# Kernel optimization log

Hardware: AMD Instinct MI355X
Metric: run time of the kernel (lower is better)

## Reference

```python
import jax, jax.numpy as jnp
import numpy as np

B, NQ, D, NH, L, P = 8, 1000, 256, 8, 4, 4
DFF = 1024
HD = D // NH
SHAPES = np.array([[128, 128], [64, 64], [32, 32], [16, 16]], dtype=np.int64)
S = int((SHAPES[:, 0] * SHAPES[:, 1]).sum())  # 21760
LEVEL_START = np.concatenate([np.zeros(1, np.int64), np.cumsum(SHAPES[:, 0] * SHAPES[:, 1])[:-1]])


def setup_inputs() -> dict:
    key = jax.random.key(0)
    ks = jax.random.split(key, 20)
    w = lambda k, shape, s=0.02: jax.random.normal(k, shape, jnp.float32) * s
    z = lambda n: jnp.zeros((n,), jnp.float32)
    return dict(
        query=w(ks[0], (B, NQ, D), 1.0),
        query_pos=w(ks[1], (B, NQ, D), 1.0),
        reference_points=jax.random.uniform(ks[2], (B, NQ, L, 4), jnp.float32),
        input_flatten=w(ks[3], (B, S, D), 1.0),
        input_spatial_shapes=SHAPES,
        input_level_start_index=LEVEL_START,
        Wq=w(ks[4], (D, D)), bq=z(D), Wk=w(ks[5], (D, D)), bk=z(D),
        Wv=w(ks[6], (D, D)), bv=z(D), Wo=w(ks[7], (D, D)), bo=z(D),
        ln1_g=jnp.ones((D,), jnp.float32), ln1_b=z(D),
        W_off=w(ks[8], (D, NH * L * P * 2)), b_off=z(NH * L * P * 2),
        W_attn=w(ks[9], (D, NH * L * P)), b_attn=z(NH * L * P),
        W_val=w(ks[10], (D, D)), b_val=z(D),
        W_cout=w(ks[11], (D, D)), b_cout=z(D),
        ln2_g=jnp.ones((D,), jnp.float32), ln2_b=z(D),
        W1=w(ks[12], (D, DFF)), b1=z(DFF),
        W2=w(ks[13], (DFF, D)), b2=z(D),
        ln3_g=jnp.ones((D,), jnp.float32), ln3_b=z(D),
    )


def layer_norm(x, g, b, eps=1e-5):
    mu = x.mean(-1, keepdims=True)
    var = ((x - mu) ** 2).mean(-1, keepdims=True)
    return (x - mu) / jnp.sqrt(var + eps) * g + b


def _ms_deform(value, shapes_np, loc, aw):
    # value: (B,S,NH,HD); loc: (B,Nq,NH,L,P,2) in [0,1]; aw: (B,Nq,NH,L,P)
    Bz, _, nh, hd = value.shape
    Nq = loc.shape[1]
    awt = aw.transpose(0, 2, 1, 3, 4)  # (B,NH,Nq,L,P)
    acc = jnp.zeros((Bz, nh, Nq, hd), value.dtype)
    start = 0
    for lvl in range(shapes_np.shape[0]):
        Hl, Wl = int(shapes_np[lvl, 0]), int(shapes_np[lvl, 1])
        vf = value[:, start:start + Hl * Wl].transpose(0, 2, 1, 3)  # (B,NH,Hl*Wl,HD)
        start += Hl * Wl
        # grid_sample align_corners=False: pixel coord = loc * size - 0.5
        lx = loc[:, :, :, lvl, :, 0].transpose(0, 2, 1, 3) * Wl - 0.5  # (B,NH,Nq,P)
        ly = loc[:, :, :, lvl, :, 1].transpose(0, 2, 1, 3) * Hl - 0.5
        x0 = jnp.floor(lx); y0 = jnp.floor(ly)
        tx = lx - x0; ty = ly - y0
        x0i = x0.astype(jnp.int32); y0i = y0.astype(jnp.int32)

        def gather(xi, yi):
            valid = (xi >= 0) & (xi < Wl) & (yi >= 0) & (yi < Hl)
            idx = jnp.clip(yi, 0, Hl - 1) * Wl + jnp.clip(xi, 0, Wl - 1)
            out = jnp.take_along_axis(vf, idx.reshape(Bz, nh, Nq * P)[..., None], axis=2)
            return out.reshape(Bz, nh, Nq, P, hd) * valid[..., None]

        g00 = gather(x0i, y0i)
        g01 = gather(x0i + 1, y0i)
        g10 = gather(x0i, y0i + 1)
        g11 = gather(x0i + 1, y0i + 1)
        samp = (g00 * ((1 - tx) * (1 - ty))[..., None] + g01 * (tx * (1 - ty))[..., None]
                + g10 * ((1 - tx) * ty)[..., None] + g11 * (tx * ty)[..., None])  # (B,NH,Nq,P,HD)
        acc = acc + jnp.einsum('bhqp,bhqpd->bhqd', awt[:, :, :, lvl], samp)
    return acc.transpose(0, 2, 1, 3).reshape(Bz, Nq, nh * hd)


def reference(query, query_pos, reference_points, input_flatten, input_spatial_shapes,
              input_level_start_index, Wq, bq, Wk, bk, Wv, bv, Wo, bo, ln1_g, ln1_b,
              W_off, b_off, W_attn, b_attn, W_val, b_val, W_cout, b_cout, ln2_g, ln2_b,
              W1, b1, W2, b2, ln3_g, ln3_b):
    Bz, Nq, Dm = query.shape
    # --- self-attention (post-norm), pos added to Q/K only ---
    qp = query + query_pos
    q = (qp @ Wq + bq).reshape(Bz, Nq, NH, HD)
    k = (qp @ Wk + bk).reshape(Bz, Nq, NH, HD)
    v = (query @ Wv + bv).reshape(Bz, Nq, NH, HD)
    att = jax.nn.softmax(jnp.einsum('bqhd,bkhd->bhqk', q, k) / jnp.sqrt(jnp.float32(HD)), axis=-1)
    sa = jnp.einsum('bhqk,bkhd->bqhd', att, v).reshape(Bz, Nq, Dm) @ Wo + bo
    x = layer_norm(query + sa, ln1_g, ln1_b)
    # --- deformable cross-attention ---
    q2 = x + query_pos
    value = (input_flatten @ W_val + b_val).reshape(Bz, -1, NH, HD)
    off = (q2 @ W_off + b_off).reshape(Bz, Nq, NH, L, P, 2)
    aw = jax.nn.softmax((q2 @ W_attn + b_attn).reshape(Bz, Nq, NH, L * P), axis=-1)
    aw = aw.reshape(Bz, Nq, NH, L, P)
    rp = reference_points  # (B,Nq,L,4) cxcywh
    loc = rp[:, :, None, :, None, :2] + off / P * rp[:, :, None, :, None, 2:] * 0.5
    shapes_np = np.asarray(input_spatial_shapes)
    ca = _ms_deform(value, shapes_np, loc, aw) @ W_cout + b_cout
    x = layer_norm(x + ca, ln2_g, ln2_b)
    # --- FFN ---
    ffn = jax.nn.relu(x @ W1 + b1) @ W2 + b2
    return layer_norm(x + ffn, ln3_g, ln3_b)
```

## Files before the change

kernel.cpp:

```cpp
#include <hip/hip_runtime.h>
#include <hip/hip_bf16.h>

#define B_   8
#define NQ_  1000
#define D_   256
#define NH_  8
#define L_   4
#define P_   4
#define DFF_ 1024
#define HD_  32
#define S_   21760
#define NTOK (B_*NQ_)

typedef short  bf16x8 __attribute__((ext_vector_type(8)));
typedef float  f32x4  __attribute__((ext_vector_type(4)));

#define WAITBAR(N) asm volatile("s_waitcnt vmcnt(" #N ") lgkmcnt(0)\n\ts_barrier" ::: "memory")
#define ENDBAR()   asm volatile("s_barrier" ::: "memory")

__device__ inline unsigned short f32_to_bf16_bits(float f) {
    unsigned int u = __float_as_uint(f);
    unsigned int rounding = 0x7FFFu + ((u >> 16) & 1u);
    u += rounding;
    return (unsigned short)(u >> 16);
}
__device__ inline float bf16_bits_to_f32(unsigned short b) {
    return __uint_as_float(((unsigned int)b) << 16);
}
__device__ inline unsigned int pack_trunc(float f0, float f1) {
    return __builtin_amdgcn_perm(__float_as_uint(f1), __float_as_uint(f0), 0x07060302u);
}
__device__ inline void async_copy16(const void* g, void* l) {
    __builtin_amdgcn_global_load_lds((const __attribute__((address_space(1))) unsigned int*)g,
                                     (__attribute__((address_space(3))) unsigned int*)l, 16, 0, 0);
}

struct PrepArgs {
    const float* wsrc[10];
    unsigned short* wdst[10];
    int wK[10], wN[10];
    const float* bq; const float* bk; const float* boff; const float* battn;
    float* qkb; float* oab;
    const float* input_flat; unsigned short* if_bf;
    const float* query; const float* qpos;
    unsigned short* q_bf; unsigned short* qp_bf;
};
__global__ __launch_bounds__(256) void prep_k(PrepArgs P)
{
    const int bid = blockIdx.x, tid = threadIdx.x;
    if (bid < 640) {
        const int job = bid >> 6, tile = bid & 63;
        const int K = P.wK[job], N = P.wN[job];
        const int tilesN = N >> 6;
        if (tile >= (K >> 6) * tilesN) return;
        const int kt = tile / tilesN, nt = tile - kt * tilesN;
        const int k0 = kt * 64, n0 = nt * 64;
        __shared__ unsigned short t_[64][65];
        const float* src = P.wsrc[job];
        unsigned short* dst = P.wdst[job];
        const int cc = tid & 63, rr = tid >> 6;
        #pragma unroll
        for (int i = 0; i < 16; i++) {
            int k = i * 4 + rr;
            t_[k][cc] = f32_to_bf16_bits(src[(size_t)(k0 + k) * N + n0 + cc]);
        }
        __syncthreads();
        #pragma unroll
        for (int i = 0; i < 16; i++) {
            int n = i * 4 + rr;
            dst[(size_t)(n0 + n) * K + k0 + cc] = t_[cc][n];
        }
    } else if (bid < 2816) {
        const int base = (bid - 640) * 2560 + tid;
        float4 fr[10][2];
        #pragma unroll
        for (int i = 0; i < 10; i++) {
            const float* p = P.input_flat + (size_t)(base + i * 256) * 8;
            fr[i][0] = *reinterpret_cast<const float4*>(p);
            fr[i][1] = *reinterpret_cast<const float4*>(p + 4);
        }
        #pragma unroll
        for (int i = 0; i < 10; i++) {
            uint4 t;
            t.x = pack_trunc(fr[i][0].x, fr[i][0].y);
            t.y = pack_trunc(fr[i][0].z, fr[i][0].w);
            t.z = pack_trunc(fr[i][1].x, fr[i][1].y);
            t.w = pack_trunc(fr[i][1].z, fr[i][1].w);
            *reinterpret_cast<uint4*>(P.if_bf + (size_t)(base + i * 256) * 8) = t;
        }
    } else if (bid == 2816) {
        P.qkb[tid]       = P.bq[tid];
        P.qkb[256 + tid] = P.bk[tid];
        P.oab[tid]       = P.boff[tid];
        if (tid < 128) P.oab[256 + tid] = P.battn[tid];
    } else {
        const int base = (bid - 2817) * 1024 + tid;
        float4 fq[4][2], fp[4][2];
        #pragma unroll
        for (int i = 0; i < 4; i++) {
            const float* q = P.query + (size_t)(base + i * 256) * 8;
            const float* p = P.qpos  + (size_t)(base + i * 256) * 8;
            fq[i][0] = *reinterpret_cast<const float4*>(q);
            fq[i][1] = *reinterpret_cast<const float4*>(q + 4);
            fp[i][0] = *reinterpret_cast<const float4*>(p);
            fp[i][1] = *reinterpret_cast<const float4*>(p + 4);
        }
        #pragma unroll
        for (int i = 0; i < 4; i++) {
            uint4 tq, tp;
            tq.x = pack_trunc(fq[i][0].x, fq[i][0].y);
            tq.y = pack_trunc(fq[i][0].z, fq[i][0].w);
            tq.z = pack_trunc(fq[i][1].x, fq[i][1].y);
            tq.w = pack_trunc(fq[i][1].z, fq[i][1].w);
            tp.x = pack_trunc(fq[i][0].x + fp[i][0].x, fq[i][0].y + fp[i][0].y);
            tp.y = pack_trunc(fq[i][0].z + fp[i][0].z, fq[i][0].w + fp[i][0].w);
            tp.z = pack_trunc(fq[i][1].x + fp[i][1].x, fq[i][1].y + fp[i][1].y);
            tp.w = pack_trunc(fq[i][1].z + fp[i][1].z, fq[i][1].w + fp[i][1].w);
            *reinterpret_cast<uint4*>(P.q_bf  + (size_t)(base + i * 256) * 8) = tq;
            *reinterpret_cast<uint4*>(P.qp_bf + (size_t)(base + i * 256) * 8) = tp;
        }
    }
}

__global__ __launch_bounds__(256) void vgemm0(const unsigned short* __restrict__ Ab,
                                              const unsigned short* __restrict__ Bt,
                                              const float* __restrict__ bias,
                                              unsigned short* __restrict__ Cb)
{
    constexpr int K = 256;
    constexpr int N = 256;
    __shared__ __align__(16) unsigned short sA[2][128 * 64];
    __shared__ __align__(16) unsigned short sB[2][128 * 64];
    const int tid = threadIdx.x;
    const int w = tid >> 6, l = tid & 63;
    const int n0 = blockIdx.x * 128, m0 = blockIdx.y * 128;
    const int wr = w >> 1, wc = w & 1;

    f32x4 acc[4][4];
    #pragma unroll
    for (int i = 0; i < 4; i++)
        #pragma unroll
        for (int j = 0; j < 4; j++)
            #pragma unroll
            for (int r = 0; r < 4; r++) acc[i][j][r] = 0.f;

    auto issueA = [&](int t, int buf) {
        #pragma unroll
        for (int r = 0; r < 4; r++) {
            int boff = ((r * 4 + w) * 64 + l) * 16;
            int row  = boff >> 7;
            int kb   = (boff & 127) ^ ((row & 7) << 4);
            async_copy16(Ab + (size_t)(m0 + row) * K + t * 64 + (kb >> 1),
                         sA[buf] + (size_t)(r * 4 + w) * 512);
        }
    };
    auto issueB = [&](int t, int buf) {
        #pragma unroll
        for (int r = 0; r < 4; r++) {
            int boff = ((r * 4 + w) * 64 + l) * 16;
            int row  = boff >> 7;
            int kb   = (boff & 127) ^ ((row & 7) << 4);
            async_copy16(Bt + (size_t)(n0 + row) * K + t * 64 + (kb >> 1),
                         sB[buf] + (size_t)(r * 4 + w) * 512);
        }
    };

    issueA(0, 0);
    issueB(0, 0);

    for (int t = 0; t < 4; t++) {
        const int cur = t & 1;
        if (t + 1 < 4) {
            issueA(t + 1, cur ^ 1);
            issueB(t + 1, cur ^ 1);
            WAITBAR(8);
        } else {
            WAITBAR(0);
        }
        #pragma unroll
        for (int kk = 0; kk < 2; kk++) {
            bf16x8 afr[4], bfr[4];
            const int kbyte = kk * 64 + ((l >> 4) << 4);
            #pragma unroll
            for (int mi = 0; mi < 4; mi++) {
                int row = wr * 64 + mi * 16 + (l & 15);
                int sw = kbyte ^ ((row & 7) << 4);
                afr[mi] = *reinterpret_cast<const bf16x8*>(&sA[cur][row * 64 + (sw >> 1)]);
            }
            #pragma unroll
            for (int ni = 0; ni < 4; ni++) {
                int row = wc * 64 + ni * 16 + (l & 15);
                int sw = kbyte ^ ((row & 7) << 4);
                bfr[ni] = *reinterpret_cast<const bf16x8*>(&sB[cur][row * 64 + (sw >> 1)]);
            }
            #pragma unroll
            for (int mi = 0; mi < 4; mi++)
                #pragma unroll
                for (int ni = 0; ni < 4; ni++)
                    acc[mi][ni] = __builtin_amdgcn_mfma_f32_16x16x32_bf16(
                        afr[mi], bfr[ni], acc[mi][ni], 0, 0, 0);
        }
        ENDBAR();
    }

    #pragma unroll
    for (int mi = 0; mi < 4; mi++) {
        #pragma unroll
        for (int ni = 0; ni < 4; ni++) {
            int col = n0 + wc * 64 + ni * 16 + (l & 15);
            float bz = bias[col];
            #pragma unroll
            for (int rg = 0; rg < 4; rg++) {
                int row = m0 + wr * 64 + mi * 16 + ((l >> 4) << 2) + rg;
                Cb[(size_t)row * N + col] = f32_to_bf16_bits(acc[mi][ni][rg] + bz);
            }
        }
    }
}

template<bool RELU, int CMODE, int BN, int K>
__global__ __launch_bounds__(256) void bgemm(const unsigned short* __restrict__ Ab,
                                             const unsigned short* __restrict__ Bt,
                                             const float* __restrict__ bias,
                                             float* __restrict__ Cf,
                                             unsigned short* __restrict__ Cb,
                                             int N)
{
    constexpr int NF   = BN / 16;
    constexpr int KF   = K / 32;
    constexpr int ROWB = K * 2;
    constexpr int FILL = BN * ROWB / 4096;

    __shared__ __align__(16) unsigned short sB[BN * K];

    const int tid = threadIdx.x;
    const int w = tid >> 6, l = tid & 63;
    const int g = l >> 4, lr = l & 15;
    const int n0 = blockIdx.x * BN;

    #pragma unroll
    for (int r = 0; r < FILL; r++) {
        int lin = (r * 256 + tid) * 16;
        int row = lin / ROWB;
        int kb  = (lin & (ROWB - 1)) ^ ((row & 7) << 4);
        async_copy16(Bt + (size_t)(n0 + row) * K + (kb >> 1), (char*)sB + lin);
    }
    asm volatile("s_waitcnt vmcnt(0)\n\ts_barrier" ::: "memory");

    float bz[NF];
    #pragma unroll
    for (int nf = 0; nf < NF; nf++) bz[nf] = bias[n0 + nf * 16 + lr];

    const int m0w = blockIdx.y * 64 + w * 16;
    const int arow = m0w + lr;

    f32x4 acc[NF];
    #pragma unroll
    for (int nf = 0; nf < NF; nf++)
        #pragma unroll
        for (int r = 0; r < 4; r++) acc[nf][r] = 0.f;

    #pragma unroll
    for (int kf = 0; kf < KF; kf++) {
        bf16x8 af = *reinterpret_cast<const bf16x8*>(Ab + (size_t)arow * K + kf * 32 + g * 8);
        #pragma unroll
        for (int nf = 0; nf < NF; nf++) {
            int brow = nf * 16 + lr;
            bf16x8 bf = *reinterpret_cast<const bf16x8*>(
                (const char*)sB + brow * ROWB + ((kf * 64 + g * 16) ^ ((brow & 7) << 4)));
            acc[nf] = __builtin_amdgcn_mfma_f32_16x16x32_bf16(af, bf, acc[nf], 0, 0, 0);
        }
    }

    #pragma unroll
    for (int nf = 0; nf < NF; nf++) {
        int col = n0 + nf * 16 + lr;
        if constexpr (CMODE == 2) {
            int row0 = m0w + g * 4;
            int bb = row0 / 1000;
            int key = row0 - bb * 1000;
            ushort4 q4;
            q4.x = f32_to_bf16_bits(acc[nf][0] + bz[nf]);
            q4.y = f32_to_bf16_bits(acc[nf][1] + bz[nf]);
            q4.z = f32_to_bf16_bits(acc[nf][2] + bz[nf]);
            q4.w = f32_to_bf16_bits(acc[nf][3] + bz[nf]);
            *reinterpret_cast<ushort4*>(Cb + (size_t)bb * 262144 + (size_t)col * 1024 + key) = q4;
        } else {
            #pragma unroll
            for (int rg = 0; rg < 4; rg++) {
                int row = m0w + g * 4 + rg;
                float v = acc[nf][rg] + bz[nf];
                if (RELU) v = fmaxf(v, 0.f);
                if constexpr (CMODE == 1)
                    Cb[(size_t)row * N + col] = f32_to_bf16_bits(v);
                else
                    Cf[(size_t)row * N + col] = v;
            }
        }
    }
}

__global__ __launch_bounds__(256) void fattn_k(const unsigned short* __restrict__ qk,
                                               const unsigned short* __restrict__ vt,
                                               unsigned short* __restrict__ sa)
{
    const int b = blockIdx.z, h = blockIdx.y;
    const int tid = threadIdx.x;
    const int w = tid >> 6, l = tid & 63;
    const int lq = l & 15, g = l >> 4;
    const int q0 = blockIdx.x * 64 + w * 16;

    __shared__ __align__(16) unsigned short Ks[2][128 * 32];
    __shared__ __align__(16) unsigned short Vs[2][32 * 128];
    __shared__ __align__(16) unsigned short Ps[4][16 * 128];

    int qrow = q0 + lq; if (qrow > NQ_ - 1) qrow = NQ_ - 1;
    const bf16x8 qfrag = *reinterpret_cast<const bf16x8*>(
        qk + ((size_t)(b * NQ_ + qrow)) * 512 + h * 32 + g * 8);

    f32x4 O0 = {0.f, 0.f, 0.f, 0.f}, O1 = {0.f, 0.f, 0.f, 0.f};
    float m = -1e30f, lsum = 0.f;
    const float scale = 0.17677669529663687f;

    const size_t kbase = (size_t)b * (NQ_ * 512) + 256 + h * 32;
    const size_t vbase = (size_t)b * 262144 + (size_t)(h * 32) * 1024;
    const int swz = (lq & 7) << 4;

    auto issueKV = [&](int kt, int buf) {
        #pragma unroll
        for (int r = 0; r < 2; r++) {
            int lin = (r * 256 + tid) * 16;
            int krow = lin >> 6;
            int kb = (lin & 63) ^ ((krow & 7) << 4);
            async_copy16(qk + kbase + (size_t)(kt * 128 + krow) * 512 + (kb >> 1),
                         (char*)Ks[buf] + lin);
            int d = lin >> 8;
            int vb = (lin & 255) ^ ((d & 7) << 4);
            async_copy16(vt + vbase + (size_t)d * 1024 + kt * 128 + (vb >> 1),
                         (char*)Vs[buf] + lin);
        }
    };

    issueKV(0, 0);

    for (int kt = 0; kt < 8; kt++) {
        const int k0 = kt * 128;
        const int cur = kt & 1;
        asm volatile("s_waitcnt vmcnt(0) lgkmcnt(0)\n\ts_barrier" ::: "memory");
        if (kt < 7) issueKV(kt + 1, cur ^ 1);

        const unsigned short* Kc = Ks[cur];
        const unsigned short* Vc = Vs[cur];

        float t[8][4];
        float tmax = -1e30f;
        const bool tail = (k0 + 128 > NQ_);
        #pragma unroll
        for (int ni = 0; ni < 8; ni++) {
            int row = ni * 16 + lq;
            bf16x8 kf = *reinterpret_cast<const bf16x8*>(
                (const char*)Kc + row * 64 + ((g * 16) ^ swz));
            f32x4 st = __builtin_amdgcn_mfma_f32_16x16x32_bf16(
                kf, qfrag, (f32x4){0.f, 0.f, 0.f, 0.f}, 0, 0, 0);
            #pragma unroll
            for (int rg = 0; rg < 4; rg++) {
                float tv = st[rg] * scale;
                if (tail) {
                    int key = k0 + ni * 16 + g * 4 + rg;
                    tv = (key < NQ_) ? tv : -1e30f;
                }
                t[ni][rg] = tv;
                tmax = fmaxf(tmax, tv);
            }
        }
        tmax = fmaxf(tmax, __shfl_xor(tmax, 16));
        tmax = fmaxf(tmax, __shfl_xor(tmax, 32));
        float mnew = fmaxf(m, tmax);
        float corr = __expf(m - mnew);
        m = mnew;

        float rs = 0.f;
        unsigned int pk[8][2];
        #pragma unroll
        for (int ni = 0; ni < 8; ni++) {
            float p0 = __expf(t[ni][0] - mnew);
            float p1 = __expf(t[ni][1] - mnew);
            float p2 = __expf(t[ni][2] - mnew);
            float p3 = __expf(t[ni][3] - mnew);
            rs += (p0 + p1) + (p2 + p3);
            pk[ni][0] = ((unsigned)f32_to_bf16_bits(p0)) | (((unsigned)f32_to_bf16_bits(p1)) << 16);
            pk[ni][1] = ((unsigned)f32_to_bf16_bits(p2)) | (((unsigned)f32_to_bf16_bits(p3)) << 16);
        }
        rs += __shfl_xor(rs, 16);
        rs += __shfl_xor(rs, 32);
        lsum = lsum * corr + rs;

        float c0 = __shfl(corr, g * 4 + 0);
        float c1 = __shfl(corr, g * 4 + 1);
        float c2 = __shfl(corr, g * 4 + 2);
        float c3 = __shfl(corr, g * 4 + 3);
        O0[0] *= c0; O0[1] *= c1; O0[2] *= c2; O0[3] *= c3;
        O1[0] *= c0; O1[1] *= c1; O1[2] *= c2; O1[3] *= c3;

        unsigned short* Pw = Ps[w];
        #pragma unroll
        for (int ni = 0; ni < 8; ni++) {
            int byteoff = lq * 256 + ((ni * 32 + g * 8) ^ swz);
            *reinterpret_cast<uint2*>((char*)Pw + byteoff) = make_uint2(pk[ni][0], pk[ni][1]);
        }

        #pragma unroll
        for (int c = 0; c < 4; c++) {
            int rb = (c * 64 + g * 16) ^ swz;
            bf16x8 pa = *reinterpret_cast<const bf16x8*>((const char*)Pw + lq * 256 + rb);
            bf16x8 v0 = *reinterpret_cast<const bf16x8*>((const char*)Vc + lq * 256 + rb);
            bf16x8 v1 = *reinterpret_cast<const bf16x8*>((const char*)Vc + (16 + lq) * 256 + rb);
            O0 = __builtin_amdgcn_mfma_f32_16x16x32_bf16(pa, v0, O0, 0, 0, 0);
            O1 = __builtin_amdgcn_mfma_f32_16x16x32_bf16(pa, v1, O1, 0, 0, 0);
        }
    }

    float linv = 1.f / lsum;
    float i0 = __shfl(linv, g * 4 + 0);
    float i1 = __shfl(linv, g * 4 + 1);
    float i2 = __shfl(linv, g * 4 + 2);
    float i3 = __shfl(linv, g * 4 + 3);
    float iv[4] = {i0, i1, i2, i3};
    #pragma unroll
    for (int rg = 0; rg < 4; rg++) {
        int qg = q0 + g * 4 + rg;
        if (qg < NQ_) {
            size_t obase = ((size_t)(b * NQ_ + qg)) * 256 + h * 32;
            sa[obase + lq]      = f32_to_bf16_bits(O0[rg] * iv[rg]);
            sa[obase + 16 + lq] = f32_to_bf16_bits(O1[rg] * iv[rg]);
        }
    }
}

template<int OM>
__global__ __launch_bounds__(256) void ln_k(const float* __restrict__ a,
                                            const float* __restrict__ bsum,
                                            const float* __restrict__ pos,
                                            const float* __restrict__ g,
                                            const float* __restrict__ be,
                                            float* __restrict__ out,
                                            unsigned short* __restrict__ outb)
{
    const int wave = threadIdx.x >> 6, lane = threadIdx.x & 63;
    const int row = blockIdx.x * 4 + wave;
    float4 xa = reinterpret_cast<const float4*>(a + (size_t)row * 256)[lane];
    float4 xb = reinterpret_cast<const float4*>(bsum + (size_t)row * 256)[lane];
    float4 x = {xa.x + xb.x, xa.y + xb.y, xa.z + xb.z, xa.w + xb.w};
    float s  = x.x + x.y + x.z + x.w;
    float ss = x.x * x.x + x.y * x.y + x.z * x.z + x.w * x.w;
    #pragma unroll
    for (int off = 32; off > 0; off >>= 1) {
        s  += __shfl_xor(s, off);
        ss += __shfl_xor(ss, off);
    }
    float mu  = s * (1.f / 256.f);
    float var = ss * (1.f / 256.f) - mu * mu;
    float rstd = rsqrtf(var + 1e-5f);
    float4 gv = reinterpret_cast<const float4*>(g)[lane];
    float4 bv = reinterpret_cast<const float4*>(be)[lane];
    float4 o = {(x.x - mu) * rstd * gv.x + bv.x,
                (x.y - mu) * rstd * gv.y + bv.y,
                (x.z - mu) * rstd * gv.z + bv.z,
                (x.w - mu) * rstd * gv.w + bv.w};
    reinterpret_cast<float4*>(out + (size_t)row * 256)[lane] = o;
    if constexpr (OM == 1) {
        ushort4 q4;
        q4.x = f32_to_bf16_bits(o.x); q4.y = f32_to_bf16_bits(o.y);
        q4.z = f32_to_bf16_bits(o.z); q4.w = f32_to_bf16_bits(o.w);
        *reinterpret_cast<ushort4*>(outb + (size_t)row * 256 + lane * 4) = q4;
    } else if constexpr (OM == 2) {
        float4 pv = reinterpret_cast<const float4*>(pos + (size_t)row * 256)[lane];
        ushort4 q4;
        q4.x = f32_to_bf16_bits(o.x + pv.x); q4.y = f32_to_bf16_bits(o.y + pv.y);
        q4.z = f32_to_bf16_bits(o.z + pv.z); q4.w = f32_to_bf16_bits(o.w + pv.w);
        *reinterpret_cast<ushort4*>(outb + (size_t)row * 256 + lane * 4) = q4;
    }
}

__device__ inline unsigned int samp2(const unsigned short* __restrict__ v,
                                     int b, int st, int Wl, int Hl,
                                     int x, int y, int hc)
{
    bool valid = (x >= 0) & (x < Wl) & (y >= 0) & (y < Hl);
    int xc = min(max(x, 0), Wl - 1);
    int yc = min(max(y, 0), Hl - 1);
    size_t idx = ((size_t)(b * S_ + st + yc * Wl + xc)) * 256 + hc;
    unsigned int val = *reinterpret_cast<const unsigned int*>(v + idx);
    return valid ? val : 0u;
}

__global__ __launch_bounds__(256) void deform_k(const float* __restrict__ rp,
                                                const float* __restrict__ oa,
                                                const unsigned short* __restrict__ value,
                                                unsigned short* __restrict__ ca)
{
    const int tk = threadIdx.x >> 7;
    const int tok = blockIdx.x * 2 + tk;
    const int b = tok / NQ_;
    const int h = (threadIdx.x >> 4) & 7;
    const int cp = threadIdx.x & 15;
    const int hc = h * 32 + cp * 2;

    const float* awp = oa + (size_t)tok * 384 + 256 + h * 16;
    float w[16];
    float mx = -1e30f;
    #pragma unroll
    for (int i = 0; i < 16; i++) { w[i] = awp[i]; mx = fmaxf(mx, w[i]); }
    float sum = 0.f;
    #pragma unroll
    for (int i = 0; i < 16; i++) { w[i] = __expf(w[i] - mx); sum += w[i]; }
    const float inv = 1.f / sum;

    const float* rpp  = rp + (size_t)tok * (L_ * 4);
    const float* offp = oa + (size_t)tok * 384 + h * 32;

    const int lvlW[4] = {128, 64, 32, 16};
    const int lvlS[4] = {0, 16384, 20480, 21504};

    float acc0 = 0.f, acc1 = 0.f;
    #pragma unroll
    for (int l = 0; l < 4; l++) {
        const int Wl = lvlW[l], Hl = lvlW[l], st = lvlS[l];
        const float cx = rpp[l * 4 + 0], cy = rpp[l * 4 + 1];
        const float cw = rpp[l * 4 + 2], chh = rpp[l * 4 + 3];
        #pragma unroll
        for (int p = 0; p < 4; p++) {
            float ox = offp[l * 8 + p * 2 + 0];
            float oy = offp[l * 8 + p * 2 + 1];
            float lx = (cx + ox * 0.25f * cw * 0.5f) * Wl - 0.5f;
            float ly = (cy + oy * 0.25f * chh * 0.5f) * Hl - 0.5f;
            float x0f = floorf(lx), y0f = floorf(ly);
            float tx = lx - x0f, ty = ly - y0f;
            int x0 = (int)x0f, y0 = (int)y0f;
            unsigned int u00 = samp2(value, b, st, Wl, Hl, x0,     y0,     hc);
            unsigned int u01 = samp2(value, b, st, Wl, Hl, x0 + 1, y0,     hc);
            unsigned int u10 = samp2(value, b, st, Wl, Hl, x0,     y0 + 1, hc);
            unsigned int u11 = samp2(value, b, st, Wl, Hl, x0 + 1, y0 + 1, hc);
            float w00 = (1.f - tx) * (1.f - ty), w01 = tx * (1.f - ty);
            float w10 = (1.f - tx) * ty,         w11 = tx * ty;
            float g0 = bf16_bits_to_f32((unsigned short)u00) * w00
                     + bf16_bits_to_f32((unsigned short)u01) * w01
                     + bf16_bits_to_f32((unsigned short)u10) * w10
                     + bf16_bits_to_f32((unsigned short)u11) * w11;
            float g1 = bf16_bits_to_f32((unsigned short)(u00 >> 16)) * w00
                     + bf16_bits_to_f32((unsigned short)(u01 >> 16)) * w01
                     + bf16_bits_to_f32((unsigned short)(u10 >> 16)) * w10
                     + bf16_bits_to_f32((unsigned short)(u11 >> 16)) * w11;
            float wa = w[l * 4 + p] * inv;
            acc0 += wa * g0;
            acc1 += wa * g1;
        }
    }
    unsigned int packed = ((unsigned)f32_to_bf16_bits(acc0)) | (((unsigned)f32_to_bf16_bits(acc1)) << 16);
    *reinterpret_cast<unsigned int*>(ca + (size_t)tok * 256 + hc) = packed;
}

extern "C" void kernel_launch(void* const* d_in, const int* in_sizes, int n_in,
                              void* d_out, int out_size, void* d_ws, size_t ws_size,
                              hipStream_t stream)
{
    const float* query      = (const float*)d_in[0];
    const float* query_pos  = (const float*)d_in[1];
    const float* ref_pts    = (const float*)d_in[2];
    const float* input_flat = (const float*)d_in[3];
    const float* Wq = (const float*)d_in[6];  const float* bq = (const float*)d_in[7];
    const float* Wk = (const float*)d_in[8];  const float* bk = (const float*)d_in[9];
    const float* Wv = (const float*)d_in[10]; const float* bv = (const float*)d_in[11];
    const float* Wo = (const float*)d_in[12]; const float* bo = (const float*)d_in[13];
    const float* ln1g = (const float*)d_in[14]; const float* ln1b = (const float*)d_in[15];
    const float* W_off = (const float*)d_in[16]; const float* b_off = (const float*)d_in[17];
    const float* W_attn = (const float*)d_in[18]; const float* b_attn = (const float*)d_in[19];
    const float* W_val = (const float*)d_in[20]; const float* b_val = (const float*)d_in[21];
    const float* W_cout = (const float*)d_in[22]; const float* b_cout = (const float*)d_in[23];
    const float* ln2g = (const float*)d_in[24]; const float* ln2b = (const float*)d_in[25];
    const float* W1 = (const float*)d_in[26]; const float* b1 = (const float*)d_in[27];
    const float* W2 = (const float*)d_in[28]; const float* b2 = (const float*)d_in[29];
    const float* ln3g = (const float*)d_in[30]; const float* ln3b = (const float*)d_in[31];
    float* out = (float*)d_out;

    char* base = (char*)d_ws;
    size_t off = 0;
    auto alloc = [&](size_t bytes) { void* p = base + off; off += (bytes + 255) & ~(size_t)255; return p; };
    unsigned short* value_bf = (unsigned short*)alloc((size_t)B_ * S_ * 256 * 2);
    unsigned short* if_bf = (unsigned short*)alloc((size_t)B_ * S_ * 256 * 2);
    unsigned short* qk_bf = (unsigned short*)alloc((size_t)NTOK * 1024 * 2);
    unsigned short* h_bf = qk_bf;
    unsigned short* vt = (unsigned short*)alloc((size_t)B_ * 256 * 1024 * 2);
    float* oa_buf = (float*)alloc((size_t)NTOK * 384 * 4);
    float* tmp0   = (float*)alloc((size_t)NTOK * 256 * 4);
    float* x1     = (float*)alloc((size_t)NTOK * 256 * 4);
    float* x2     = (float*)alloc((size_t)NTOK * 256 * 4);
    unsigned short* sc_bf  = (unsigned short*)alloc((size_t)NTOK * 256 * 2);
    unsigned short* q_bf   = (unsigned short*)alloc((size_t)NTOK * 256 * 2);
    unsigned short* qp_bf  = (unsigned short*)alloc((size_t)NTOK * 256 * 2);
    unsigned short* x1p_bf = (unsigned short*)alloc((size_t)NTOK * 256 * 2);
    unsigned short* x2_bf  = (unsigned short*)alloc((size_t)NTOK * 256 * 2);
    unsigned short* wqk   = (unsigned short*)alloc(512 * 256 * 2);
    unsigned short* wv    = (unsigned short*)alloc(256 * 256 * 2);
    unsigned short* wo    = (unsigned short*)alloc(256 * 256 * 2);
    unsigned short* woa   = (unsigned short*)alloc(384 * 256 * 2);
    unsigned short* wval  = (unsigned short*)alloc(256 * 256 * 2);
    unsigned short* wcout = (unsigned short*)alloc(256 * 256 * 2);
    unsigned short* w1t   = (unsigned short*)alloc(1024 * 256 * 2);
    unsigned short* w2t   = (unsigned short*)alloc(256 * 1024 * 2);
    float* qkbias = (float*)alloc(512 * 4);
    float* oabias = (float*)alloc(384 * 4);

    dim3 blk(256);

    PrepArgs P;
    P.wsrc[0] = Wq;    P.wdst[0] = wqk;               P.wK[0] = 256;  P.wN[0] = 256;
    P.wsrc[1] = Wk;    P.wdst[1] = wqk + 256 * 256;   P.wK[1] = 256;  P.wN[1] = 256;
    P.wsrc[2] = Wv;    P.wdst[2] = wv;                P.wK[2] = 256;  P.wN[2] = 256;
    P.wsrc[3] = Wo;    P.wdst[3] = wo;                P.wK[3] = 256;  P.wN[3] = 256;
    P.wsrc[4] = W_off; P.wdst[4] = woa;               P.wK[4] = 256;  P.wN[4] = 256;
    P.wsrc[5] = W_attn;P.wdst[5] = woa + 256 * 256;   P.wK[5] = 256;  P.wN[5] = 128;
    P.wsrc[6] = W_val; P.wdst[6] = wval;              P.wK[6] = 256;  P.wN[6] = 256;
    P.wsrc[7] = W_cout;P.wdst[7] = wcout;             P.wK[7] = 256;  P.wN[7] = 256;
    P.wsrc[8] = W1;    P.wdst[8] = w1t;               P.wK[8] = 256;  P.wN[8] = 1024;
    P.wsrc[9] = W2;    P.wdst[9] = w2t;               P.wK[9] = 1024; P.wN[9] = 256;
    P.bq = bq; P.bk = bk; P.boff = b_off; P.battn = b_attn;
    P.qkb = qkbias; P.oab = oabias;
    P.input_flat = input_flat; P.if_bf = if_bf;
    P.query = query; P.qpos = query_pos; P.q_bf = q_bf; P.qp_bf = qp_bf;
    prep_k<<<3067, blk, 0, stream>>>(P);

    bgemm<false, 1,  64, 256><<<dim3(8, 125), blk, 0, stream>>>(qp_bf, wqk, qkbias, nullptr, qk_bf, 512);
    bgemm<false, 2,  64, 256><<<dim3(4, 125), blk, 0, stream>>>(q_bf,  wv,  bv,     nullptr, vt,    256);
    fattn_k<<<dim3(16, NH_, B_), blk, 0, stream>>>(qk_bf, vt, sc_bf);
    bgemm<false, 0,  64, 256><<<dim3(4, 125), blk, 0, stream>>>(sc_bf, wo, bo, tmp0, nullptr, 256);
    ln_k<2><<<NTOK / 4, blk, 0, stream>>>(query, tmp0, query_pos, ln1g, ln1b, x1, x1p_bf);

    vgemm0<<<dim3(2, 1360), blk, 0, stream>>>(if_bf, wval, b_val, value_bf);
    bgemm<false, 0,  64, 256><<<dim3(6, 125), blk, 0, stream>>>(x1p_bf, woa, oabias, oa_buf, nullptr, 384);
    deform_k<<<NTOK / 2, blk, 0, stream>>>(ref_pts, oa_buf, value_bf, sc_bf);
    bgemm<false, 0,  64, 256><<<dim3(4, 125), blk, 0, stream>>>(sc_bf, wcout, b_cout, tmp0, nullptr, 256);
    ln_k<1><<<NTOK / 4, blk, 0, stream>>>(x1, tmp0, nullptr, ln2g, ln2b, x2, x2_bf);

    bgemm<true,  1,  64, 256><<<dim3(16, 125), blk, 0, stream>>>(x2_bf, w1t, b1, nullptr, h_bf, 1024);
    bgemm<false, 0,  32, 1024><<<dim3(8, 125), blk, 0, stream>>>(h_bf, w2t, b2, tmp0, nullptr, 256);
    ln_k<0><<<NTOK / 4, blk, 0, stream>>>(x2, tmp0, nullptr, ln3g, ln3b, out, nullptr);
}
```

Before: 276.0 us.

## Fuse fp32-to-bf16 conversion of input_flatten into the value-projection GEMM

Measured after the change: 253.7 us. -8.1%, faster.

```diff
diff --git a/kernel.cpp b/kernel.cpp
--- a/kernel.cpp
+++ b/kernel.cpp
@@ -41,7 +41,6 @@
     int wK[10], wN[10];
     const float* bq; const float* bk; const float* boff; const float* battn;
     float* qkb; float* oab;
-    const float* input_flat; unsigned short* if_bf;
     const float* query; const float* qpos;
     unsigned short* q_bf; unsigned short* qp_bf;
 };
@@ -70,31 +69,13 @@
             int n = i * 4 + rr;
             dst[(size_t)(n0 + n) * K + k0 + cc] = t_[cc][n];
         }
-    } else if (bid < 2816) {
-        const int base = (bid - 640) * 2560 + tid;
-        float4 fr[10][2];
-        #pragma unroll
-        for (int i = 0; i < 10; i++) {
-            const float* p = P.input_flat + (size_t)(base + i * 256) * 8;
-            fr[i][0] = *reinterpret_cast<const float4*>(p);
-            fr[i][1] = *reinterpret_cast<const float4*>(p + 4);
-        }
-        #pragma unroll
-        for (int i = 0; i < 10; i++) {
-            uint4 t;
-            t.x = pack_trunc(fr[i][0].x, fr[i][0].y);
-            t.y = pack_trunc(fr[i][0].z, fr[i][0].w);
-            t.z = pack_trunc(fr[i][1].x, fr[i][1].y);
-            t.w = pack_trunc(fr[i][1].z, fr[i][1].w);
-            *reinterpret_cast<uint4*>(P.if_bf + (size_t)(base + i * 256) * 8) = t;
-        }
-    } else if (bid == 2816) {
+    } else if (bid == 640) {
         P.qkb[tid]       = P.bq[tid];
         P.qkb[256 + tid] = P.bk[tid];
         P.oab[tid]       = P.boff[tid];
         if (tid < 128) P.oab[256 + tid] = P.battn[tid];
     } else {
-        const int base = (bid - 2817) * 1024 + tid;
+        const int base = (bid - 641) * 1024 + tid;
         float4 fq[4][2], fp[4][2];
         #pragma unroll
         for (int i = 0; i < 4; i++) {
@@ -122,19 +103,20 @@
     }
 }
 
-__global__ __launch_bounds__(256) void vgemm0(const unsigned short* __restrict__ Ab,
+__global__ __launch_bounds__(256) void vgemmF(const float* __restrict__ Af,
                                               const unsigned short* __restrict__ Bt,
                                               const float* __restrict__ bias,
                                               unsigned short* __restrict__ Cb)
 {
     constexpr int K = 256;
     constexpr int N = 256;
-    __shared__ __align__(16) unsigned short sA[2][128 * 64];
-    __shared__ __align__(16) unsigned short sB[2][128 * 64];
+    __shared__ __align__(16) float          sA[2][128 * 32];
+    __shared__ __align__(16) unsigned short sB[2][128 * 32];
     const int tid = threadIdx.x;
     const int w = tid >> 6, l = tid & 63;
     const int n0 = blockIdx.x * 128, m0 = blockIdx.y * 128;
     const int wr = w >> 1, wc = w & 1;
+    const int lq = l & 15, g = l >> 4;
 
     f32x4 acc[4][4];
     #pragma unroll
@@ -147,59 +129,64 @@
     auto issueA = [&](int t, int buf) {
         #pragma unroll
         for (int r = 0; r < 4; r++) {
-            int boff = ((r * 4 + w) * 64 + l) * 16;
-            int row  = boff >> 7;
-            int kb   = (boff & 127) ^ ((row & 7) << 4);
-            async_copy16(Ab + (size_t)(m0 + row) * K + t * 64 + (kb >> 1),
-                         sA[buf] + (size_t)(r * 4 + w) * 512);
+            int lin = (r * 256 + tid) * 16;
+            int row = lin >> 7;
+            int kb  = (lin & 127) ^ ((row & 3) << 5);
+            async_copy16(Af + (size_t)(m0 + row) * K + t * 32 + (kb >> 2),
+                         (char*)sA[buf] + lin);
         }
     };
     auto issueB = [&](int t, int buf) {
         #pragma unroll
-        for (int r = 0; r < 4; r++) {
-            int boff = ((r * 4 + w) * 64 + l) * 16;
-            int row  = boff >> 7;
-            int kb   = (boff & 127) ^ ((row & 7) << 4);
-            async_copy16(Bt + (size_t)(n0 + row) * K + t * 64 + (kb >> 1),
-                         sB[buf] + (size_t)(r * 4 + w) * 512);
+        for (int r = 0; r < 2; r++) {
+            int lin = (r * 256 + tid) * 16;
+            int row = lin >> 6;
+            int kb  = (lin & 63) ^ ((row & 3) << 4);
+            async_copy16(Bt + (size_t)(n0 + row) * K + t * 32 + (kb >> 1),
+                         (char*)sB[buf] + lin);
         }
     };
 
     issueA(0, 0);
     issueB(0, 0);
 
-    for (int t = 0; t < 4; t++) {
+    for (int t = 0; t < 8; t++) {
         const int cur = t & 1;
-        if (t + 1 < 4) {
+        if (t + 1 < 8) {
             issueA(t + 1, cur ^ 1);
             issueB(t + 1, cur ^ 1);
-            WAITBAR(8);
+            WAITBAR(6);
         } else {
             WAITBAR(0);
         }
-        #pragma unroll
-        for (int kk = 0; kk < 2; kk++) {
-            bf16x8 afr[4], bfr[4];
-            const int kbyte = kk * 64 + ((l >> 4) << 4);
+
+        bf16x8 afr[4], bfr[4];
+        #pragma unroll
+        for (int mi = 0; mi < 4; mi++) {
+            int row = wr * 64 + mi * 16 + lq;
+            int off = (g * 32) ^ ((row & 3) << 5);
+            const char* p = (const char*)sA[cur] + row * 128 + off;
+            float4 a0 = *reinterpret_cast<const float4*>(p);
+            float4 a1 = *reinterpret_cast<const float4*>(p + 16);
+            uint4 u;
+            u.x = pack_trunc(a0.x, a0.y);
+            u.y = pack_trunc(a0.z, a0.w);
+            u.z = pack_trunc(a1.x, a1.y);
+            u.w = pack_trunc(a1.z, a1.w);
+            afr[mi] = *reinterpret_cast<bf16x8*>(&u);
+        }
+        #pragma unroll
+        for (int ni = 0; ni < 4; ni++) {
+            int row = wc * 64 + ni * 16 + lq;
+            int off = (g * 16) ^ ((row & 3) << 4);
+            bfr[ni] = *reinterpret_cast<const bf16x8*>((const char*)sB[cur] + row * 64 + off);
+        }
+        #pragma unroll
+        for (int mi = 0; mi < 4; mi++)
             #pragma unroll
-            for (int mi = 0; mi < 4; mi++) {
-                int row = wr * 64 + mi * 16 + (l & 15);
-                int sw = kbyte ^ ((row & 7) << 4);
-                afr[mi] = *reinterpret_cast<const bf16x8*>(&sA[cur][row * 64 + (sw >> 1)]);
-            }
-            #pragma unroll
-            for (int ni = 0; ni < 4; ni++) {
-                int row = wc * 64 + ni * 16 + (l & 15);
-                int sw = kbyte ^ ((row & 7) << 4);
-                bfr[ni] = *reinterpret_cast<const bf16x8*>(&sB[cur][row * 64 + (sw >> 1)]);
-            }
-            #pragma unroll
-            for (int mi = 0; mi < 4; mi++)
-                #pragma unroll
-                for (int ni = 0; ni < 4; ni++)
-                    acc[mi][ni] = __builtin_amdgcn_mfma_f32_16x16x32_bf16(
-                        afr[mi], bfr[ni], acc[mi][ni], 0, 0, 0);
-        }
+            for (int ni = 0; ni < 4; ni++)
+                acc[mi][ni] = __builtin_amdgcn_mfma_f32_16x16x32_bf16(
+                    afr[mi], bfr[ni], acc[mi][ni], 0, 0, 0);
         ENDBAR();
     }
 
@@ -207,11 +194,11 @@
     for (int mi = 0; mi < 4; mi++) {
         #pragma unroll
         for (int ni = 0; ni < 4; ni++) {
-            int col = n0 + wc * 64 + ni * 16 + (l & 15);
+            int col = n0 + wc * 64 + ni * 16 + lq;
             float bz = bias[col];
             #pragma unroll
             for (int rg = 0; rg < 4; rg++) {
-                int row = m0 + wr * 64 + mi * 16 + ((l >> 4) << 2) + rg;
+                int row = m0 + wr * 64 + mi * 16 + g * 4 + rg;
                 Cb[(size_t)row * N + col] = f32_to_bf16_bits(acc[mi][ni][rg] + bz);
             }
         }
@@ -587,7 +574,6 @@
     size_t off = 0;
     auto alloc = [&](size_t bytes) { void* p = base + off; off += (bytes + 255) & ~(size_t)255; return p; };
     unsigned short* value_bf = (unsigned short*)alloc((size_t)B_ * S_ * 256 * 2);
-    unsigned short* if_bf = (unsigned short*)alloc((size_t)B_ * S_ * 256 * 2);
     unsigned short* qk_bf = (unsigned short*)alloc((size_t)NTOK * 1024 * 2);
     unsigned short* h_bf = qk_bf;
     unsigned short* vt = (unsigned short*)alloc((size_t)B_ * 256 * 1024 * 2);
@@ -626,9 +612,8 @@
     P.wsrc[9] = W2;    P.wdst[9] = w2t;               P.wK[9] = 1024; P.wN[9] = 256;
     P.bq = bq; P.bk = bk; P.boff = b_off; P.battn = b_attn;
     P.qkb = qkbias; P.oab = oabias;
-    P.input_flat = input_flat; P.if_bf = if_bf;
     P.query = query; P.qpos = query_pos; P.q_bf = q_bf; P.qp_bf = qp_bf;
-    prep_k<<<3067, blk, 0, stream>>>(P);
+    prep_k<<<891, blk, 0, stream>>>(P);
 
     bgemm<false, 1,  64, 256><<<dim3(8, 125), blk, 0, stream>>>(qp_bf, wqk, qkbias, nullptr, qk_bf, 512);
     bgemm<false, 2,  64, 256><<<dim3(4, 125), blk, 0, stream>>>(q_bf,  wv,  bv,     nullptr, vt,    256);
@@ -636,7 +621,7 @@
     bgemm<false, 0,  64, 256><<<dim3(4, 125), blk, 0, stream>>>(sc_bf, wo, bo, tmp0, nullptr, 256);
     ln_k<2><<<NTOK / 4, blk, 0, stream>>>(query, tmp0, query_pos, ln1g, ln1b, x1, x1p_bf);
 
-    vgemm0<<<dim3(2, 1360), blk, 0, stream>>>(if_bf, wval, b_val, value_bf);
+    vgemmF<<<dim3(2, 1360), blk, 0, stream>>>(input_flat, wval, b_val, value_bf);
     bgemm<false, 0,  64, 256><<<dim3(6, 125), blk, 0, stream>>>(x1p_bf, woa, oabias, oa_buf, nullptr, 384);
     deform_k<<<NTOK / 2, blk, 0, stream>>>(ref_pts, oa_buf, value_bf, sc_bf);
     bgemm<false, 0,  64, 256><<<dim3(4, 125), blk, 0, stream>>>(sc_bf, wcout, b_cout, tmp0, nullptr, 256);
```
